# Kernel optimization log

Measured on AMD Instinct MI355X. Metric: run time of the kernel, lower is better.

## Reference

```python
import jax, jax.numpy as jnp
import numpy as np

B, L, D, H, NL, FF, W, V = 4, 8192, 256, 4, 4, 1024, 512, 14
DH = D // H


def _ln(x, g, b, eps=1e-5):
    m = jnp.mean(x, axis=-1, keepdims=True)
    v = jnp.mean((x - m) ** 2, axis=-1, keepdims=True)
    return (x - m) / jnp.sqrt(v + eps) * g + b


def setup_inputs() -> dict:
    key = jax.random.key(0)
    ks = jax.random.split(key, 12)
    s = 0.02
    inp = {
        "byte_ids": jax.random.randint(ks[0], (B, L), 0, V, dtype=jnp.int32),
        "embed": jax.random.normal(ks[1], (V, D), jnp.float32) * s,
        "wq": jax.random.normal(ks[2], (NL, D, D), jnp.float32) * s,
        "bq": jnp.zeros((NL, D), jnp.float32),
        "wk": jax.random.normal(ks[3], (NL, D, D), jnp.float32) * s,
        "bk": jnp.zeros((NL, D), jnp.float32),
        "wv": jax.random.normal(ks[4], (NL, D, D), jnp.float32) * s,
        "bv": jnp.zeros((NL, D), jnp.float32),
        "wo": jax.random.normal(ks[5], (NL, D, D), jnp.float32) * s,
        "bo": jnp.zeros((NL, D), jnp.float32),
        "ln1_g": jnp.ones((NL, D), jnp.float32),
        "ln1_b": jnp.zeros((NL, D), jnp.float32),
        "ln2_g": jnp.ones((NL, D), jnp.float32),
        "ln2_b": jnp.zeros((NL, D), jnp.float32),
        "w1": jax.random.normal(ks[6], (NL, D, FF), jnp.float32) * s,
        "b1": jnp.zeros((NL, FF), jnp.float32),
        "w2": jax.random.normal(ks[7], (NL, FF, D), jnp.float32) * s,
        "b2": jnp.zeros((NL, D), jnp.float32),
        "lnf_g": jnp.ones((D,), jnp.float32),
        "lnf_b": jnp.zeros((D,), jnp.float32),
        "head_w": jax.random.normal(ks[8], (D, V), jnp.float32) * s,
    }
    return inp


def _forward(byte_ids, embed, wq, bq, wk, bk, wv, bv, wo, bo,
             ln1_g, ln1_b, ln2_g, ln2_b, w1, b1, w2, b2, lnf_g, lnf_b, head_w):
    x = embed[byte_ids]                      # [B, L, D]
    nb = L // W                              # number of 512-wide blocks
    scale = 1.0 / np.sqrt(DH)
    # ALiBi slopes: 2^(-8h/H) for h = 1..H
    slopes = jnp.exp2(-8.0 * jnp.arange(1, H + 1, dtype=jnp.float32) / H)
    qi = jnp.arange(W)[:, None]
    ki = jnp.arange(2 * W)[None, :]
    dist = (W + qi - ki).astype(jnp.float32)            # i - j for kv window [prev, cur]
    base = (dist >= 0) & (dist <= W)                    # causal sliding window (left=512)
    mask = jnp.broadcast_to(base, (nb, W, 2 * W))
    mask = mask.at[0].set(base & (ki >= W))             # first block has no previous block
    bias = -slopes[:, None, None] * dist                # [H, W, 2W]

    for l in range(NL):
        h = _ln(x, ln1_g[l], ln1_b[l])
        q = (h @ wq[l] + bq[l]).reshape(B, nb, W, H, DH)
        k = (h @ wk[l] + bk[l]).reshape(B, nb, W, H, DH)
        v = (h @ wv[l] + bv[l]).reshape(B, nb, W, H, DH)
        kp = jnp.pad(k, ((0, 0), (1, 0), (0, 0), (0, 0), (0, 0)))[:, :nb]
        vp = jnp.pad(v, ((0, 0), (1, 0), (0, 0), (0, 0), (0, 0)))[:, :nb]
        kk = jnp.concatenate([kp, k], axis=2)           # [B, nb, 2W, H, DH]
        vv = jnp.concatenate([vp, v], axis=2)
        s = jnp.einsum('bnqhd,bnkhd->bhnqk', q, kk) * scale + bias[None, :, None]
        s = jnp.where(mask[None, None], s, -1e9)
        p = jax.nn.softmax(s, axis=-1)                  # [B, H, nb, W, 2W]
        o = jnp.einsum('bhnqk,bnkhd->bnqhd', p, vv).reshape(B, L, D)
        x = x + o @ wo[l] + bo[l]
        h2 = _ln(x, ln2_g[l], ln2_b[l])
        x = x + jax.nn.gelu(h2 @ w1[l] + b1[l]) @ w2[l] + b2[l]
    x = _ln(x, lnf_g, lnf_b)
    return x @ head_w                                   # [B, L, V]


def reference(byte_ids, embed, wq, bq, wk, bk, wv, bv, wo, bo,
              ln1_g, ln1_b, ln2_g, ln2_b, w1, b1, w2, b2, lnf_g, lnf_b, head_w):
    return _forward(byte_ids, embed, wq, bq, wk, bk, wv, bv, wo, bo,
                    ln1_g, ln1_b, ln2_g, ln2_b, w1, b1, w2, b2, lnf_g, lnf_b, head_w)
```

## Files before the change

### kernel.cpp

```cpp
#include <hip/hip_runtime.h>

#define NLAYER 4
#define M_TOK 32768

typedef unsigned short u16;
typedef __bf16 bf16x8 __attribute__((ext_vector_type(8)));
typedef float f32x4 __attribute__((ext_vector_type(4)));

__device__ inline float bf2f(u16 u) {
    union { unsigned int i; float f; } x; x.i = ((unsigned int)u) << 16; return x.f;
}
__device__ inline u16 f2bf(float f) {
    union { float f; unsigned int i; } x; x.f = f;
    return (u16)((x.i + 0x8000u) >> 16);
}
__device__ inline bf16x8 ld_frag(const u16* p) {
    union { uint4 u; bf16x8 b; } c; c.u = *(const uint4*)p; return c.b;
}
__device__ inline unsigned pk2(float a, float b) {
    union { float f; unsigned i; } ua, ub; ua.f = a; ub.f = b;
    return __builtin_amdgcn_perm(ub.i + 0x8000u, ua.i + 0x8000u, 0x07060302u);
}
__device__ inline float gelu_f(float x) {
    float z = 0.7978845608028654f * (x + 0.044715f * x * x * x);
    float t = 1.f - 2.f / (__expf(2.f * z) + 1.f);
    return 0.5f * x * (1.f + t);
}
__device__ inline void gload_lds16(const u16* g, u16* l) {
    __builtin_amdgcn_global_load_lds(
        (const __attribute__((address_space(1))) unsigned int*)g,
        (__attribute__((address_space(3))) unsigned int*)l, 16, 0, 0);
}

#define BAR()   asm volatile("s_barrier" ::: "memory")
#define WAIT4() asm volatile("s_waitcnt vmcnt(4)" ::: "memory")
#define WAIT0() asm volatile("s_waitcnt vmcnt(0)" ::: "memory")
#define LGKM0() asm volatile("s_waitcnt lgkmcnt(0)" ::: "memory")

__global__ void sniff_kernel(const u16* __restrict__ raw, int* __restrict__ flag)
{
    if (threadIdx.x == 0 && blockIdx.x == 0) {
        int ok = 1;
        for (int i = 0; i < 32; i++) {
            u16 u = raw[i];
            int e = (u >> 7) & 0xFF;
            if (!(u == 0 || (e >= 90 && e <= 140))) ok = 0;
        }
        *flag = ok;
    }
}

struct IngestArgs { const void* src[20]; int off[21]; };
__global__ __launch_bounds__(256) void ingest_all(
    IngestArgs a, float* __restrict__ dst, const int* __restrict__ flag, int tot)
{
    int gid = blockIdx.x * 256 + threadIdx.x;
    if (gid >= tot) return;
    int lo = 0, hi = 20;
    while (hi - lo > 1) { int mid = (lo + hi) >> 1; if (gid >= a.off[mid]) lo = mid; else hi = mid; }
    int local = gid - a.off[lo];
    if (*flag) dst[gid] = bf2f(((const u16*)a.src[lo])[local]);
    else       dst[gid] = ((const float*)a.src[lo])[local];
}

__global__ __launch_bounds__(256) void pack_qkv(
    const float* __restrict__ wq, const float* __restrict__ wk, const float* __restrict__ wv,
    const float* __restrict__ bq, const float* __restrict__ bk, const float* __restrict__ bv,
    u16* __restrict__ wT, float* __restrict__ bT)
{
    int l = blockIdx.y;
    int idx = blockIdx.x * 256 + threadIdx.x;
    int n = idx >> 8, k = idx & 255;
    const float* w = (n < 256) ? wq : (n < 512) ? wk : wv;
    int nn = n & 255;
    wT[(size_t)l * 768 * 256 + idx] = f2bf(w[(size_t)l * 65536 + k * 256 + nn]);
    if (idx < 768) {
        const float* bb = (idx < 256) ? bq : (idx < 512) ? bk : bv;
        bT[l * 768 + idx] = bb[l * 256 + (idx & 255)];
    }
}

__global__ __launch_bounds__(256) void pack_t(
    const float* __restrict__ src, u16* __restrict__ dst, int R, int C)
{
    int l = blockIdx.y;
    int idx = blockIdx.x * 256 + threadIdx.x;
    int c = idx / R, r = idx % R;
    size_t base = (size_t)l * R * C;
    dst[base + idx] = f2bf(src[base + (size_t)r * C + c]);
}

__global__ __launch_bounds__(256) void embed_kernel(
    const int* __restrict__ ids, const float* __restrict__ emb, float* __restrict__ x)
{
    int t = blockIdx.x * 256 + threadIdx.x;
    int row = t >> 6, c = (t & 63) * 4;
    int id = ids[row];
    float4 e = *(const float4*)(emb + (size_t)id * 256 + c);
    *(float4*)(x + (size_t)row * 256 + c) = e;
}

__global__ __launch_bounds__(256) void ln_kernel(
    const float* __restrict__ x, const float* __restrict__ g, const float* __restrict__ b,
    u16* __restrict__ out)
{
    int row = blockIdx.x * 4 + (threadIdx.x >> 6);
    int lane = threadIdx.x & 63;
    float4 v = *(const float4*)(x + (size_t)row * 256 + lane * 4);
    float s = v.x + v.y + v.z + v.w;
    float s2 = v.x * v.x + v.y * v.y + v.z * v.z + v.w * v.w;
    #pragma unroll
    for (int mk = 1; mk < 64; mk <<= 1) {
        s += __shfl_xor(s, mk, 64);
        s2 += __shfl_xor(s2, mk, 64);
    }
    float mean = s * (1.f / 256.f);
    float var = s2 * (1.f / 256.f) - mean * mean;
    float rstd = rsqrtf(var + 1e-5f);
    int d0 = lane * 4;
    float4 gg = *(const float4*)(g + d0);
    float4 bb = *(const float4*)(b + d0);
    union { unsigned long long u; u16 q[4]; } oo;
    oo.q[0] = f2bf((v.x - mean) * rstd * gg.x + bb.x);
    oo.q[1] = f2bf((v.y - mean) * rstd * gg.y + bb.y);
    oo.q[2] = f2bf((v.z - mean) * rstd * gg.z + bb.z);
    oo.q[3] = f2bf((v.w - mean) * rstd * gg.w + bb.w);
    *(unsigned long long*)(out + (size_t)row * 256 + d0) = oo.u;
}

template <int EPI, int K>
__global__ __launch_bounds__(256, 3) void gemm_db(
    const u16* __restrict__ A, const u16* __restrict__ Bt, const float* __restrict__ bias,
    u16* __restrict__ outB, float* __restrict__ resid, int N)
{
    __shared__ u16 lds[17408];
    constexpr int NC = K / 32;
    int tid = threadIdx.x, lane = tid & 63, wave = tid >> 6;
    int col = lane & 15, quad = lane >> 4;
    int wm = (wave >> 1) * 64, wn = (wave & 1) * 64;
    int bm = blockIdx.x * 128, bn = blockIdx.y * 128;

    u16* A0 = lds;          u16* A1 = lds + 4096;
    u16* B0 = lds + 8192;   u16* B1 = lds + 12288;

    int rL = wave * 32 + (lane >> 2);
    int sx = (lane & 3) ^ ((lane >> 2) & 3);
    const u16* srcA0 = A + (size_t)(bm + rL) * K + sx * 8;
    const u16* srcB0 = Bt + (size_t)(bn + rL) * K + sx * 8;
    int st = wave * 1024 + lane * 8;

    int g8 = (quad ^ (col & 3)) * 8;
    int aoff = (wm + col) * 32 + g8;
    int boff = (wn + col) * 32 + g8;

    f32x4 z4 = { 0.f, 0.f, 0.f, 0.f };
    f32x4 acc[4][4];
    #pragma unroll
    for (int i = 0; i < 4; i++)
        #pragma unroll
        for (int j = 0; j < 4; j++) acc[i][j] = z4;

    #define STAGE(c, Ax, Bx) do {                                        \
        const u16* _a = srcA0 + (c) * 32;                                \
        const u16* _b = srcB0 + (c) * 32;                                \
        gload_lds16(_a, (Ax) + st);                                      \
        gload_lds16(_a + (size_t)16 * K, (Ax) + st + 512);               \
        gload_lds16(_b, (Bx) + st);                                      \
        gload_lds16(_b + (size_t)16 * K, (Bx) + st + 512);               \
    } while (0)

    #define CHUNK(Ax, Bx) do {                                           \
        bf16x8 af[4], bfv[4];                                            \
        _Pragma("unroll")                                                \
        for (int i = 0; i < 4; i++) af[i] = ld_frag((Ax) + aoff + i * 512); \
        _Pragma("unroll")                                                \
        for (int j = 0; j < 4; j++) bfv[j] = ld_frag((Bx) + boff + j * 512); \
        _Pragma("unroll")                                                \
        for (int i = 0; i < 4; i++)                                      \
            _Pragma("unroll")                                            \
            for (int j = 0; j < 4; j++)                                  \
                acc[i][j] = __builtin_amdgcn_mfma_f32_16x16x32_bf16(af[i], bfv[j], acc[i][j], 0, 0, 0); \
    } while (0)

    STAGE(0, A0, B0);
    for (int c = 0; c < NC - 2; c += 2) {
        STAGE(c + 1, A1, B1);
        WAIT4(); BAR();
        CHUNK(A0, B0);
        LGKM0(); BAR();
        STAGE(c + 2, A0, B0);
        WAIT4(); BAR();
        CHUNK(A1, B1);
        LGKM0(); BAR();
    }
    STAGE(NC - 1, A1, B1);
    WAIT4(); BAR();
    CHUNK(A0, B0);
    LGKM0(); BAR();
    WAIT0(); BAR();
    CHUNK(A1, B1);
    __syncthreads();

    if (EPI == 2) {
        float* Cf = (float*)lds;
        #pragma unroll
        for (int h = 0; h < 2; h++) {
            if ((wave & 1) == h) {
                #pragma unroll
                for (int j = 0; j < 4; j++) {
                    float bv = bias[bn + wn + j * 16 + col];
                    #pragma unroll
                    for (int i = 0; i < 4; i++) {
                        int rl = wm + i * 16 + quad * 4;
                        #pragma unroll
                        for (int r = 0; r < 4; r++)
                            Cf[(rl + r) * 68 + j * 16 + col] = acc[i][j][r] + bv;
                    }
                }
            }
            LGKM0(); BAR();
            #pragma unroll
            for (int u = 0; u < 8; u++) {
                int row = u * 16 + (tid >> 4);
                int cseg = (tid & 15) * 4;
                float* rp = resid + (size_t)(bm + row) * N + bn + h * 64 + cseg;
                const float* cp = Cf + row * 68 + cseg;
                float4 rv = *(float4*)rp;
                float4 cv = *(const float4*)cp;
                rv.x += cv.x; rv.y += cv.y; rv.z += cv.z; rv.w += cv.w;
                *(float4*)rp = rv;
            }
            LGKM0(); BAR();
        }
    } else {
        u16* Cs = lds;
        #pragma unroll
        for (int j = 0; j < 4; j++) {
            int ccl = wn + j * 16 + col;
            float bv = bias[bn + ccl];
            #pragma unroll
            for (int i = 0; i < 4; i++) {
                int rl = wm + i * 16 + quad * 4;
                #pragma unroll
                for (int r = 0; r < 4; r++) {
                    float v = acc[i][j][r] + bv;
                    if (EPI == 1) v = gelu_f(v);
                    Cs[(rl + r) * 136 + ccl] = f2bf(v);
                }
            }
        }
        __syncthreads();
        #pragma unroll
        for (int u = 0; u < 8; u++) {
            int row = u * 16 + (tid >> 4);
            int c8 = (tid & 15) * 8;
            u16* op = outB + (size_t)(bm + row) * N + bn + c8;
            *(uint4*)op = *(const uint4*)(Cs + row * 136 + c8);
        }
    }
    #undef STAGE
    #undef CHUNK
}

__global__ __launch_bounds__(256, 3) void attn_kernel(
    const u16* __restrict__ qkv, u16* __restrict__ attno)
{
    __shared__ u16 Ks[64 * 72];
    __shared__ u16 Vt[64 * 68];
    __shared__ u16 Ps[4 * 16 * 72];
    int g = blockIdx.x;
    int xc = g & 7, t = g >> 3;
    int r12 = t & 15, s8 = t >> 4;
    int ng = s8 * 8 + xc;
    int bb = ng >> 4, nn = ng & 15;
    int hh = r12 & 3, t2 = r12 >> 2;
    int tid = threadIdx.x, lane = tid & 63, wave = tid >> 6;
    int q16 = lane & 15, quad = lane >> 4;
    float slope = exp2f(-2.f * (float)(hh + 1));
    float slopeL = slope * 1.44269504f;
    const float C1 = 0.125f * 1.44269504f;

    int qt0 = t2 * 2;
    size_t tok0 = (size_t)bb * 8192 + nn * 512;

    bf16x8 bqf[2][2];
    {
        int qrow = t2 * 128 + wave * 16 + q16;
        const u16* qp = qkv + (tok0 + qrow) * 768 + hh * 64 + quad * 8;
        bqf[0][0] = ld_frag(qp);
        bqf[0][1] = ld_frag(qp + 32);
        const u16* qp1 = qp + (size_t)64 * 768;
        bqf[1][0] = ld_frag(qp1);
        bqf[1][1] = ld_frag(qp1 + 32);
    }

    f32x4 z4 = { 0.f, 0.f, 0.f, 0.f };
    f32x4 oa[2][4];
    #pragma unroll
    for (int s = 0; s < 2; s++)
        #pragma unroll
        for (int dt = 0; dt < 4; dt++) oa[s][dt] = z4;
    float lsum[2] = { 0.f, 0.f };
    u16* Psw = Ps + wave * (16 * 72);

    int c_lo = (nn == 0) ? 8 : qt0;
    int c_hi = qt0 + 9;

    int kkK = tid >> 3, c8k = (tid & 7) * 8;
    int kk2 = (tid & 31) * 2, c8v = (tid >> 5) * 8;

    uint4 pk0, pk1, pv0, pv1;
    auto load_c = [&](int c) {
        int tok = (int)tok0 - 512 + c * 64;
        const u16* bK = qkv + (size_t)(tok + kkK) * 768 + hh * 64 + 256 + c8k;
        pk0 = *(const uint4*)bK;
        pk1 = *(const uint4*)(bK + (size_t)32 * 768);
        const u16* bV = qkv + (size_t)(tok + kk2) * 768 + hh * 64 + 512 + c8v;
        pv0 = *(const uint4*)bV;
        pv1 = *(const uint4*)(bV + 768);
    };
    load_c(c_lo);

    for (int c = c_lo; c <= c_hi; ++c) {
        LGKM0(); BAR();
        *(uint4*)(Ks + kkK * 72 + c8k) = pk0;
        *(uint4*)(Ks + (kkK + 32) * 72 + c8k) = pk1;
        {
            union { uint4 u; u16 s[8]; } a, b;
            a.u = pv0; b.u = pv1;
            #pragma unroll
            for (int j = 0; j < 8; j++) {
                unsigned w = (unsigned)a.s[j] | ((unsigned)b.s[j] << 16);
                *(unsigned*)(Vt + (c8v + j) * 68 + kk2) = w;
            }
        }
        if (c < c_hi) load_c(c + 1);
        LGKM0(); BAR();

        bf16x8 kf[4][2];
        #pragma unroll
        for (int kt = 0; kt < 4; kt++)
            #pragma unroll
            for (int ks = 0; ks < 2; ks++)
                kf[kt][ks] = ld_frag(Ks + (kt * 16 + q16) * 72 + ks * 32 + quad * 8);
        bf16x8 vf[4][2];
        #pragma unroll
        for (int dt = 0; dt < 4; dt++)
            #pragma unroll
            for (int ks = 0; ks < 2; ks++) {
                union { uint2 p[2]; bf16x8 b; } cv;
                const u16* vp = Vt + (dt * 16 + q16) * 68 + ks * 32 + quad * 8;
                cv.p[0] = *(const uint2*)(vp);
                cv.p[1] = *(const uint2*)(vp + 4);
                vf[dt][ks] = cv.b;
            }

        int act0 = (c <= qt0 + 8);
        int act1 = (c >= qt0 + 1);
        #pragma unroll
        for (int s = 0; s < 2; s++) {
            if (s == 0 ? !act0 : !act1) continue;
            f32x4 st[4];
            #pragma unroll
            for (int kt = 0; kt < 4; kt++) {
                f32x4 z = z4;
                #pragma unroll
                for (int ks = 0; ks < 2; ks++)
                    z = __builtin_amdgcn_mfma_f32_16x16x32_bf16(kf[kt][ks], bqf[s][ks], z, 0, 0, 0);
                st[kt] = z;
            }
            int qg = t2 * 128 + s * 64 + wave * 16 + q16;
            int D = 512 + qg - c * 64 - quad * 4;
            float nb = -slopeL * (float)D;
            int qts = qt0 + s;
            int diag = (c == qts) || (c == qts + 8);
            float ls = 0.f;
            #pragma unroll
            for (int kt = 0; kt < 4; kt++) {
                float pk[4];
                #pragma unroll
                for (int r = 0; r < 4; r++) {
                    float bias = fmaf(slopeL, (float)(kt * 16 + r), nb);
                    float p = exp2f(fmaf(st[kt][r], C1, bias));
                    if (diag) {
                        int dd = D - (kt * 16 + r);
                        p = ((unsigned)dd <= 512u) ? p : 0.f;
                    }
                    ls += p; pk[r] = p;
                }
                uint2 w;
                w.x = pk2(pk[0], pk[1]);
                w.y = pk2(pk[2], pk[3]);
                *(uint2*)(Psw + q16 * 72 + kt * 16 + quad * 4) = w;
            }
            lsum[s] += ls;
            bf16x8 pf[2];
            #pragma unroll
            for (int ks = 0; ks < 2; ks++)
                pf[ks] = ld_frag(Psw + q16 * 72 + ks * 32 + quad * 8);
            #pragma unroll
            for (int dt = 0; dt < 4; dt++)
                #pragma unroll
                for (int ks = 0; ks < 2; ks++)
                    oa[s][dt] = __builtin_amdgcn_mfma_f32_16x16x32_bf16(pf[ks], vf[dt][ks], oa[s][dt], 0, 0, 0);
        }
    }

    #pragma unroll
    for (int s = 0; s < 2; s++) {
        float lr = lsum[s];
        lr += __shfl_xor(lr, 16, 64);
        lr += __shfl_xor(lr, 32, 64);
        lsum[s] = lr;
    }
    float* lx = (float*)Psw;
    if (quad == 0) { lx[q16] = lsum[0]; lx[16 + q16] = lsum[1]; }
    #pragma unroll
    for (int s = 0; s < 2; s++) {
        float4 lq = *(const float4*)(lx + s * 16 + quad * 4);
        float inv[4] = { 1.f / lq.x, 1.f / lq.y, 1.f / lq.z, 1.f / lq.w };
        int tokb = (int)tok0 + t2 * 128 + s * 64 + wave * 16 + quad * 4;
        #pragma unroll
        for (int r = 0; r < 4; r++)
            #pragma unroll
            for (int dt = 0; dt < 4; dt++)
                attno[(size_t)(tokb + r) * 256 + hh * 64 + dt * 16 + q16] = f2bf(oa[s][dt][r] * inv[r]);
    }
}

__global__ __launch_bounds__(256) void head_ln_kernel(
    const float* __restrict__ x, const float* __restrict__ g, const float* __restrict__ b,
    const float* __restrict__ hw, const int* __restrict__ flag,
    u16* __restrict__ outb, float* __restrict__ outf)
{
    __shared__ float Wt[14 * 256];
    int tid = threadIdx.x;
    for (int i = tid; i < 14 * 256; i += 256) {
        int v = i >> 8, d = i & 255;
        Wt[i] = hw[d * 14 + v];
    }
    __syncthreads();
    int wave = tid >> 6, lane = tid & 63;
    int row = blockIdx.x * 4 + wave;
    float4 v = *(const float4*)(x + (size_t)row * 256 + lane * 4);
    float s = v.x + v.y + v.z + v.w;
    float s2 = v.x * v.x + v.y * v.y + v.z * v.z + v.w * v.w;
    #pragma unroll
    for (int mk = 1; mk < 64; mk <<= 1) {
        s += __shfl_xor(s, mk, 64);
        s2 += __shfl_xor(s2, mk, 64);
    }
    float mean = s * (1.f / 256.f);
    float var = s2 * (1.f / 256.f) - mean * mean;
    float rstd = rsqrtf(var + 1e-5f);
    int d0 = lane * 4;
    float4 gg = *(const float4*)(g + d0);
    float4 bb = *(const float4*)(b + d0);
    float hv[4];
    hv[0] = (v.x - mean) * rstd * gg.x + bb.x;
    hv[1] = (v.y - mean) * rstd * gg.y + bb.y;
    hv[2] = (v.z - mean) * rstd * gg.z + bb.z;
    hv[3] = (v.w - mean) * rstd * gg.w + bb.w;
    int isbf = *flag;
    for (int vv = 0; vv < 14; vv++) {
        float4 wv4 = *(const float4*)(Wt + vv * 256 + lane * 4);
        float sd = hv[0] * wv4.x + hv[1] * wv4.y + hv[2] * wv4.z + hv[3] * wv4.w;
        #pragma unroll
        for (int mk = 1; mk < 64; mk <<= 1) sd += __shfl_xor(sd, mk, 64);
        if (lane == 0) {
            if (isbf) outb[(size_t)row * 14 + vv] = f2bf(sd);
            else      outf[(size_t)row * 14 + vv] = sd;
        }
    }
}

extern "C" void kernel_launch(void* const* d_in, const int* in_sizes, int n_in,
                              void* d_out, int out_size, void* d_ws, size_t ws_size,
                              hipStream_t stream) {
    (void)out_size; (void)ws_size;
    const int* ids = (const int*)d_in[0];

    char* ws = (char*)d_ws;
    int* flag = (int*)ws; ws += 16;

    IngestArgs ia;
    int off = 0;
    for (int i = 1; i < n_in && i <= 20; i++) {
        ia.src[i - 1] = d_in[i];
        ia.off[i - 1] = off;
        off += in_sizes[i];
    }
    ia.off[20] = off;
    float* fbase = (float*)ws;
    ws += (size_t)((off + 3) & ~3) * 4;
    float* fin[21];
    for (int i = 1; i <= 20; i++) fin[i] = fbase + ia.off[i - 1];

    float* x    = (float*)ws;  ws += (size_t)M_TOK * 256 * 4;
    u16* h      = (u16*)ws;    ws += (size_t)M_TOK * 256 * 2;
    u16* qkv    = (u16*)ws;    ws += (size_t)M_TOK * 768 * 2;
    u16* attno  = (u16*)ws;    ws += (size_t)M_TOK * 256 * 2;
    u16* ff     = (u16*)ws;    ws += (size_t)M_TOK * 1024 * 2;
    u16* wqkvT  = (u16*)ws;    ws += (size_t)NLAYER * 768 * 256 * 2;
    u16* woT    = (u16*)ws;    ws += (size_t)NLAYER * 256 * 256 * 2;
    u16* w1T    = (u16*)ws;    ws += (size_t)NLAYER * 1024 * 256 * 2;
    u16* w2T    = (u16*)ws;    ws += (size_t)NLAYER * 256 * 1024 * 2;
    float* bqkv = (float*)ws;  ws += (size_t)NLAYER * 768 * 4;

    sniff_kernel<<<1, 64, 0, stream>>>((const u16*)d_in[1], flag);
    ingest_all<<<(off + 255) / 256, 256, 0, stream>>>(ia, fbase, flag, off);

    pack_qkv<<<dim3(768, NLAYER), 256, 0, stream>>>(fin[2], fin[4], fin[6],
                                                    fin[3], fin[5], fin[7], wqkvT, bqkv);
    pack_t<<<dim3(256, NLAYER), 256, 0, stream>>>(fin[8], woT, 256, 256);
    pack_t<<<dim3(1024, NLAYER), 256, 0, stream>>>(fin[14], w1T, 256, 1024);
    pack_t<<<dim3(1024, NLAYER), 256, 0, stream>>>(fin[16], w2T, 1024, 256);

    embed_kernel<<<8192, 256, 0, stream>>>(ids, fin[1], x);

    for (int l = 0; l < NLAYER; ++l) {
        ln_kernel<<<8192, 256, 0, stream>>>(x, fin[10] + l * 256, fin[11] + l * 256, h);
        gemm_db<0, 256><<<dim3(256, 6), 256, 0, stream>>>(h, wqkvT + (size_t)l * 768 * 256,
                                                          bqkv + l * 768, qkv, nullptr, 768);
        attn_kernel<<<1024, 256, 0, stream>>>(qkv, attno);
        gemm_db<2, 256><<<dim3(256, 2), 256, 0, stream>>>(attno, woT + (size_t)l * 65536,
                                                          fin[9] + l * 256, nullptr, x, 256);
        ln_kernel<<<8192, 256, 0, stream>>>(x, fin[12] + l * 256, fin[13] + l * 256, h);
        gemm_db<1, 256><<<dim3(256, 8), 256, 0, stream>>>(h, w1T + (size_t)l * 262144,
                                                          fin[15] + l * 1024, ff, nullptr, 1024);
        gemm_db<2, 1024><<<dim3(256, 2), 256, 0, stream>>>(ff, w2T + (size_t)l * 262144,
                                                           fin[17] + l * 256, nullptr, x, 256);
    }
    head_ln_kernel<<<8192, 256, 0, stream>>>(x, fin[18], fin[19], fin[20], flag,
                                             (u16*)d_out, (float*)d_out);
}
```

Before: 1.050 ms.

## Replace LDS double-buffered GEMM with direct global-to-register fragment loads

```diff
diff --git a/kernel.cpp b/kernel.cpp
--- a/kernel.cpp
+++ b/kernel.cpp
@@ -26,15 +26,8 @@
     float t = 1.f - 2.f / (__expf(2.f * z) + 1.f);
     return 0.5f * x * (1.f + t);
 }
-__device__ inline void gload_lds16(const u16* g, u16* l) {
-    __builtin_amdgcn_global_load_lds(
-        (const __attribute__((address_space(1))) unsigned int*)g,
-        (__attribute__((address_space(3))) unsigned int*)l, 16, 0, 0);
-}
 
 #define BAR()   asm volatile("s_barrier" ::: "memory")
-#define WAIT4() asm volatile("s_waitcnt vmcnt(4)" ::: "memory")
-#define WAIT0() asm volatile("s_waitcnt vmcnt(0)" ::: "memory")
 #define LGKM0() asm volatile("s_waitcnt lgkmcnt(0)" ::: "memory")
 
 __global__ void sniff_kernel(const u16* __restrict__ raw, int* __restrict__ flag)
@@ -129,29 +122,24 @@
 }
 
 template <int EPI, int K>
-__global__ __launch_bounds__(256, 3) void gemm_db(
+__global__ __launch_bounds__(256, 3) void gemm_reg(
     const u16* __restrict__ A, const u16* __restrict__ Bt, const float* __restrict__ bias,
     u16* __restrict__ outB, float* __restrict__ resid, int N)
 {
     __shared__ u16 lds[17408];
-    constexpr int NC = K / 32;
     int tid = threadIdx.x, lane = tid & 63, wave = tid >> 6;
     int col = lane & 15, quad = lane >> 4;
     int wm = (wave >> 1) * 64, wn = (wave & 1) * 64;
     int bm = blockIdx.x * 128, bn = blockIdx.y * 128;
 
-    u16* A0 = lds;          u16* A1 = lds + 4096;
-    u16* B0 = lds + 8192;   u16* B1 = lds + 12288;
-
-    int rL = wave * 32 + (lane >> 2);
-    int sx = (lane & 3) ^ ((lane >> 2) & 3);
-    const u16* srcA0 = A + (size_t)(bm + rL) * K + sx * 8;
-    const u16* srcB0 = Bt + (size_t)(bn + rL) * K + sx * 8;
-    int st = wave * 1024 + lane * 8;
-
-    int g8 = (quad ^ (col & 3)) * 8;
-    int aoff = (wm + col) * 32 + g8;
-    int boff = (wn + col) * 32 + g8;
+    const u16* ap[4];
+    const u16* bp[4];
+    #pragma unroll
+    for (int i = 0; i < 4; i++)
+        ap[i] = A + (size_t)(bm + wm + i * 16 + col) * K + quad * 8;
+    #pragma unroll
+    for (int j = 0; j < 4; j++)
+        bp[j] = Bt + (size_t)(bn + wn + j * 16 + col) * K + quad * 8;
 
     f32x4 z4 = { 0.f, 0.f, 0.f, 0.f };
     f32x4 acc[4][4];
@@ -160,46 +148,19 @@
         #pragma unroll
         for (int j = 0; j < 4; j++) acc[i][j] = z4;
 
-    #define STAGE(c, Ax, Bx) do {                                        \
-        const u16* _a = srcA0 + (c) * 32;                                \
-        const u16* _b = srcB0 + (c) * 32;                                \
-        gload_lds16(_a, (Ax) + st);                                      \
-        gload_lds16(_a + (size_t)16 * K, (Ax) + st + 512);               \
-        gload_lds16(_b, (Bx) + st);                                      \
-        gload_lds16(_b + (size_t)16 * K, (Bx) + st + 512);               \
-    } while (0)
-
-    #define CHUNK(Ax, Bx) do {                                           \
-        bf16x8 af[4], bfv[4];                                            \
-        _Pragma("unroll")                                                \
-        for (int i = 0; i < 4; i++) af[i] = ld_frag((Ax) + aoff + i * 512); \
-        _Pragma("unroll")                                                \
-        for (int j = 0; j < 4; j++) bfv[j] = ld_frag((Bx) + boff + j * 512); \
-        _Pragma("unroll")                                                \
-        for (int i = 0; i < 4; i++)                                      \
-            _Pragma("unroll")                                            \
-            for (int j = 0; j < 4; j++)                                  \
-                acc[i][j] = __builtin_amdgcn_mfma_f32_16x16x32_bf16(af[i], bfv[j], acc[i][j], 0, 0, 0); \
-    } while (0)
-
-    STAGE(0, A0, B0);
-    for (int c = 0; c < NC - 2; c += 2) {
-        STAGE(c + 1, A1, B1);
-        WAIT4(); BAR();
-        CHUNK(A0, B0);
-        LGKM0(); BAR();
-        STAGE(c + 2, A0, B0);
-        WAIT4(); BAR();
-        CHUNK(A1, B1);
-        LGKM0(); BAR();
-    }
-    STAGE(NC - 1, A1, B1);
-    WAIT4(); BAR();
-    CHUNK(A0, B0);
-    LGKM0(); BAR();
-    WAIT0(); BAR();
-    CHUNK(A1, B1);
-    __syncthreads();
+    #pragma unroll
+    for (int ks = 0; ks < K / 32; ks++) {
+        bf16x8 af[4], bfv[4];
+        #pragma unroll
+        for (int i = 0; i < 4; i++) af[i] = ld_frag(ap[i] + ks * 32);
+        #pragma unroll
+        for (int j = 0; j < 4; j++) bfv[j] = ld_frag(bp[j] + ks * 32);
+        #pragma unroll
+        for (int i = 0; i < 4; i++)
+            #pragma unroll
+            for (int j = 0; j < 4; j++)
+                acc[i][j] = __builtin_amdgcn_mfma_f32_16x16x32_bf16(af[i], bfv[j], acc[i][j], 0, 0, 0);
+    }
 
     if (EPI == 2) {
         float* Cf = (float*)lds;
@@ -258,8 +219,6 @@
             *(uint4*)op = *(const uint4*)(Cs + row * 136 + c8);
         }
     }
-    #undef STAGE
-    #undef CHUNK
 }
 
 __global__ __launch_bounds__(256, 3) void attn_kernel(
@@ -520,16 +479,16 @@
 
     for (int l = 0; l < NLAYER; ++l) {
         ln_kernel<<<8192, 256, 0, stream>>>(x, fin[10] + l * 256, fin[11] + l * 256, h);
-        gemm_db<0, 256><<<dim3(256, 6), 256, 0, stream>>>(h, wqkvT + (size_t)l * 768 * 256,
-                                                          bqkv + l * 768, qkv, nullptr, 768);
+        gemm_reg<0, 256><<<dim3(256, 6), 256, 0, stream>>>(h, wqkvT + (size_t)l * 768 * 256,
+                                                           bqkv + l * 768, qkv, nullptr, 768);
         attn_kernel<<<1024, 256, 0, stream>>>(qkv, attno);
-        gemm_db<2, 256><<<dim3(256, 2), 256, 0, stream>>>(attno, woT + (size_t)l * 65536,
-                                                          fin[9] + l * 256, nullptr, x, 256);
+        gemm_reg<2, 256><<<dim3(256, 2), 256, 0, stream>>>(attno, woT + (size_t)l * 65536,
+                                                           fin[9] + l * 256, nullptr, x, 256);
         ln_kernel<<<8192, 256, 0, stream>>>(x, fin[12] + l * 256, fin[13] + l * 256, h);
-        gemm_db<1, 256><<<dim3(256, 8), 256, 0, stream>>>(h, w1T + (size_t)l * 262144,
-                                                          fin[15] + l * 1024, ff, nullptr, 1024);
-        gemm_db<2, 1024><<<dim3(256, 2), 256, 0, stream>>>(ff, w2T + (size_t)l * 262144,
-                                                           fin[17] + l * 256, nullptr, x, 256);
+        gemm_reg<1, 256><<<dim3(256, 8), 256, 0, stream>>>(h, w1T + (size_t)l * 262144,
+                                                           fin[15] + l * 1024, ff, nullptr, 1024);
+        gemm_reg<2, 1024><<<dim3(256, 2), 256, 0, stream>>>(ff, w2T + (size_t)l * 262144,
+                                                            fin[17] + l * 256, nullptr, x, 256);
     }
     head_ln_kernel<<<8192, 256, 0, stream>>>(x, fin[18], fin[19], fin[20], flag,
                                              (u16*)d_out, (float*)d_out);
```

Result: slower. 1.350 ms (+28.6%).

## Fuse FFN up-projection, GELU and down-projection into one MLP kernel

Applied to the files above, without the earlier changes.

```diff
diff --git a/kernel.cpp b/kernel.cpp
--- a/kernel.cpp
+++ b/kernel.cpp
@@ -260,6 +260,169 @@
     }
     #undef STAGE
     #undef CHUNK
+}
+
+__global__ __launch_bounds__(512, 2) void mlp_kernel(
+    const u16* __restrict__ Ain, const u16* __restrict__ w1T, const u16* __restrict__ w2T,
+    const float* __restrict__ b1, const float* __restrict__ b2, float* __restrict__ xr)
+{
+    __shared__ u16 As[32768];
+    __shared__ u16 Ws[32768];
+    __shared__ u16 Gs[16384];
+
+    int tid = threadIdx.x, lane = tid & 63, wave = tid >> 6;
+    int col = lane & 15, quad = lane >> 4;
+    int wq = wave & 3, wh = wave >> 2;
+    int wm2 = wh * 64;
+    int bm = blockIdx.x * 128;
+    int g8 = (quad ^ (col & 3)) * 8;
+    int gx8 = (col & 7) * 8;
+    int sx = (lane & 3) ^ ((lane >> 2) & 3);
+    int st = wave * 512 + lane * 8;
+    int aoffB = (wm2 + col) * 32 + g8;
+    int bw1off = (wq * 16 + col) * 32 + g8;
+    int wn2off = (wq * 64 + col) * 32 + g8;
+    int wn1c = wq * 16 + col;
+
+    float b1r[16], b2r[4];
+    {
+        int c0 = wq * 16 + col;
+        #pragma unroll
+        for (int f = 0; f < 8; f++) {
+            b1r[f * 2 + 0] = b1[f * 128 + c0];
+            b1r[f * 2 + 1] = b1[f * 128 + 64 + c0];
+        }
+        #pragma unroll
+        for (int j = 0; j < 4; j++) b2r[j] = b2[wq * 64 + j * 16 + col];
+    }
+
+    f32x4 z4 = { 0.f, 0.f, 0.f, 0.f };
+    f32x4 acc2[4][4];
+    #pragma unroll
+    for (int i = 0; i < 4; i++)
+        #pragma unroll
+        for (int j = 0; j < 4; j++) acc2[i][j] = z4;
+
+    #define STAGE_W1(ff, hh, WB) do {                                               \
+        const u16* _s = w1T + (size_t)((ff) * 128 + (hh) * 64 + wq * 16 + (lane >> 2)) * 256 + sx * 8; \
+        _Pragma("unroll")                                                           \
+        for (int i_ = 0; i_ < 4; i_++)                                              \
+            gload_lds16(_s + (i_ * 2 + wh) * 32, (WB) + i_ * 4096 + st);            \
+    } while (0)
+
+    #define STAGE_W2(ff, kh, WB) do {                                               \
+        _Pragma("unroll")                                                           \
+        for (int i_ = 0; i_ < 4; i_++) {                                            \
+            int _rv = (i_ & 1) * 128 + wave * 16 + (lane >> 2);                     \
+            gload_lds16(w2T + (size_t)_rv * 1024 + (ff) * 128 + (kh) * 64 + (i_ >> 1) * 32 + sx * 8, \
+                        (WB) + (i_ >> 1) * 8192 + (i_ & 1) * 4096 + st);            \
+        }                                                                           \
+    } while (0)
+
+    #define G1_PHASE(ff, hh, WB) do {                                               \
+        f32x4 a1[4]; a1[0] = z4; a1[1] = z4; a1[2] = z4; a1[3] = z4;                \
+        _Pragma("unroll")                                                           \
+        for (int ks = 0; ks < 8; ks++) {                                            \
+            bf16x8 bw = ld_frag((WB) + ks * 2048 + bw1off);                         \
+            _Pragma("unroll")                                                       \
+            for (int i = 0; i < 4; i++) {                                           \
+                bf16x8 av = ld_frag(As + ks * 4096 + aoffB + i * 512);              \
+                a1[i] = __builtin_amdgcn_mfma_f32_16x16x32_bf16(av, bw, a1[i], 0, 0, 0); \
+            }                                                                       \
+        }                                                                           \
+        float bv = b1r[(ff) * 2 + (hh)];                                            \
+        _Pragma("unroll")                                                           \
+        for (int i = 0; i < 4; i++) {                                               \
+            _Pragma("unroll")                                                       \
+            for (int r = 0; r < 4; r++) {                                           \
+                int row = wm2 + i * 16 + quad * 4 + r;                              \
+                float vv = gelu_f(a1[i][r] + bv);                                   \
+                Gs[row * 128 + (((hh) * 64 + wn1c) ^ ((row & 7) * 8))] = f2bf(vv);  \
+            }                                                                       \
+        }                                                                           \
+    } while (0)
+
+    #define G2_PHASE(kh, WB) do {                                                   \
+        _Pragma("unroll")                                                           \
+        for (int ks = 0; ks < 2; ks++) {                                            \
+            bf16x8 gf[4], wf[4];                                                    \
+            _Pragma("unroll")                                                       \
+            for (int i = 0; i < 4; i++)                                             \
+                gf[i] = ld_frag(Gs + (wm2 + i * 16 + col) * 128 +                   \
+                                (((kh) * 64 + ks * 32 + quad * 8) ^ gx8));          \
+            _Pragma("unroll")                                                       \
+            for (int j = 0; j < 4; j++)                                             \
+                wf[j] = ld_frag((WB) + ks * 8192 + wn2off + j * 512);               \
+            _Pragma("unroll")                                                       \
+            for (int i = 0; i < 4; i++)                                             \
+                _Pragma("unroll")                                                   \
+                for (int j = 0; j < 4; j++)                                         \
+                    acc2[i][j] = __builtin_amdgcn_mfma_f32_16x16x32_bf16(gf[i], wf[j], acc2[i][j], 0, 0, 0); \
+        }                                                                           \
+    } while (0)
+
+    {
+        const u16* sA = Ain + (size_t)(bm + wave * 16 + (lane >> 2)) * 256 + sx * 8;
+        #pragma unroll
+        for (int c = 0; c < 8; c++) gload_lds16(sA + c * 32, As + c * 4096 + st);
+    }
+    STAGE_W1(0, 0, Ws);
+    STAGE_W1(0, 1, Ws + 16384);
+    WAIT4(); BAR();
+
+    for (int f = 0; f < 8; ++f) {
+        G1_PHASE(f, 0, Ws);
+        LGKM0(); BAR();
+        STAGE_W2(f, 0, Ws);
+        WAIT4(); BAR();
+        G1_PHASE(f, 1, Ws + 16384);
+        LGKM0(); BAR();
+        STAGE_W2(f, 1, Ws + 16384);
+        WAIT4(); BAR();
+        G2_PHASE(0, Ws);
+        BAR();
+        if (f < 7) { STAGE_W1(f + 1, 0, Ws); WAIT4(); } else WAIT0();
+        BAR();
+        G2_PHASE(1, Ws + 16384);
+        BAR();
+        if (f < 7) { STAGE_W1(f + 1, 1, Ws + 16384); WAIT4(); }
+        BAR();
+    }
+
+    float* Cf = (float*)As;
+    #pragma unroll
+    for (int h = 0; h < 4; h++) {
+        if (wq == h) {
+            #pragma unroll
+            for (int j = 0; j < 4; j++) {
+                float bv = b2r[j];
+                #pragma unroll
+                for (int i = 0; i < 4; i++) {
+                    int rl = wm2 + i * 16 + quad * 4;
+                    #pragma unroll
+                    for (int r = 0; r < 4; r++)
+                        Cf[(rl + r) * 68 + j * 16 + col] = acc2[i][j][r] + bv;
+                }
+            }
+        }
+        LGKM0(); BAR();
+        #pragma unroll
+        for (int u = 0; u < 4; u++) {
+            int row = u * 32 + (tid >> 4);
+            int cseg = (tid & 15) * 4;
+            float* rp = xr + (size_t)(bm + row) * 256 + h * 64 + cseg;
+            const float* cp = Cf + row * 68 + cseg;
+            float4 rv = *(float4*)rp;
+            float4 cv = *(const float4*)cp;
+            rv.x += cv.x; rv.y += cv.y; rv.z += cv.z; rv.w += cv.w;
+            *(float4*)rp = rv;
+        }
+        LGKM0(); BAR();
+    }
+    #undef STAGE_W1
+    #undef STAGE_W2
+    #undef G1_PHASE
+    #undef G2_PHASE
 }
 
 __global__ __launch_bounds__(256, 3) void attn_kernel(
@@ -500,7 +663,6 @@
     u16* h      = (u16*)ws;    ws += (size_t)M_TOK * 256 * 2;
     u16* qkv    = (u16*)ws;    ws += (size_t)M_TOK * 768 * 2;
     u16* attno  = (u16*)ws;    ws += (size_t)M_TOK * 256 * 2;
-    u16* ff     = (u16*)ws;    ws += (size_t)M_TOK * 1024 * 2;
     u16* wqkvT  = (u16*)ws;    ws += (size_t)NLAYER * 768 * 256 * 2;
     u16* woT    = (u16*)ws;    ws += (size_t)NLAYER * 256 * 256 * 2;
     u16* w1T    = (u16*)ws;    ws += (size_t)NLAYER * 1024 * 256 * 2;
@@ -526,10 +688,9 @@
         gemm_db<2, 256><<<dim3(256, 2), 256, 0, stream>>>(attno, woT + (size_t)l * 65536,
                                                           fin[9] + l * 256, nullptr, x, 256);
         ln_kernel<<<8192, 256, 0, stream>>>(x, fin[12] + l * 256, fin[13] + l * 256, h);
-        gemm_db<1, 256><<<dim3(256, 8), 256, 0, stream>>>(h, w1T + (size_t)l * 262144,
-                                                          fin[15] + l * 1024, ff, nullptr, 1024);
-        gemm_db<2, 1024><<<dim3(256, 2), 256, 0, stream>>>(ff, w2T + (size_t)l * 262144,
-                                                           fin[17] + l * 256, nullptr, x, 256);
+        mlp_kernel<<<256, 512, 0, stream>>>(h, w1T + (size_t)l * 262144,
+                                            w2T + (size_t)l * 262144,
+                                            fin[15] + l * 1024, fin[17] + l * 256, x);
     }
     head_ln_kernel<<<8192, 256, 0, stream>>>(x, fin[18], fin[19], fin[20], flag,
                                              (u16*)d_out, (float*)d_out);
```

Result: faster. 983.8 us (-6.3%).

## Fuse MLP up and down projections into a producer-consumer kernel

Applied to the files above, without the earlier changes.

```diff
diff --git a/kernel.cpp b/kernel.cpp
--- a/kernel.cpp
+++ b/kernel.cpp
@@ -260,6 +260,143 @@
     }
     #undef STAGE
     #undef CHUNK
+}
+
+__global__ __launch_bounds__(1024, 4) void mlp_pc(
+    const u16* __restrict__ hin, const u16* __restrict__ w1T, const u16* __restrict__ w2T,
+    const float* __restrict__ b1, const float* __restrict__ b2, float* __restrict__ xr)
+{
+    __shared__ u16 L[81920];
+    int tid = threadIdx.x, lane = tid & 63, wave = tid >> 6;
+    int colL = lane & 15, quad = lane >> 4;
+    int sx = (lane & 3) ^ ((lane >> 2) & 3);
+    int bm = blockIdx.x * 128;
+    int isG1 = (wave < 8);
+
+    int c0 = wave >> 2;
+    int nb1 = (wave & 3) * 16;
+    const u16* w1s = w1T + (size_t)(nb1 + (lane >> 2)) * 256 + sx * 8;
+    int w1d = c0 * 2048 + nb1 * 32 + lane * 8;
+    const u16* w2s = w2T + (size_t)(wave * 16 + (lane >> 2)) * 1024 + sx * 8;
+    int w2d = wave * 512 + lane * 8;
+
+    int wnh = wave & 1, wmg = (wave >> 1) & 3;
+    int gw = wave & 7, gr = gw >> 2, gc = gw & 3;
+    int swzA = (quad ^ (colL & 3)) * 8;
+
+    f32x4 z4 = { 0.f, 0.f, 0.f, 0.f };
+    f32x4 acc2[4][4];
+    #pragma unroll
+    for (int i = 0; i < 4; i++)
+        #pragma unroll
+        for (int j = 0; j < 4; j++) acc2[i][j] = z4;
+
+    #define STAGE_W1(ff, base) do {                                   \
+        const u16* _s = w1s + (size_t)(ff) * 16384;                   \
+        gload_lds16(_s + c0 * 32, L + (base) + w1d);                  \
+        gload_lds16(_s + (c0 + 4) * 32, L + (base) + 8192 + w1d);     \
+    } while (0)
+
+    #define STAGE_W2(ff, base) do {                                   \
+        const u16* _s = w2s + (ff) * 64;                              \
+        gload_lds16(_s, L + (base) + w2d);                            \
+        gload_lds16(_s + 32, L + (base) + 8192 + w2d);                \
+    } while (0)
+
+    #define G2_BODY(gbase, wbase) do {                                               \
+        const u16* _g = L + (gbase);                                                 \
+        const u16* _w = L + (wbase);                                                 \
+        _Pragma("unroll")                                                            \
+        for (int ks = 0; ks < 2; ks++) {                                             \
+            bf16x8 gf[4], wf[4];                                                     \
+            _Pragma("unroll")                                                        \
+            for (int i = 0; i < 4; i++) {                                            \
+                int row = gr * 64 + i * 16 + colL;                                   \
+                gf[i] = ld_frag(_g + row * 64 + (((ks * 4 + quad) ^ (colL & 7)) * 8)); \
+            }                                                                        \
+            _Pragma("unroll")                                                        \
+            for (int j = 0; j < 4; j++)                                              \
+                wf[j] = ld_frag(_w + ks * 8192 + (gc * 64 + j * 16 + colL) * 32 + swzA); \
+            _Pragma("unroll")                                                        \
+            for (int i = 0; i < 4; i++)                                              \
+                _Pragma("unroll")                                                    \
+                for (int j = 0; j < 4; j++)                                          \
+                    acc2[i][j] = __builtin_amdgcn_mfma_f32_16x16x32_bf16(gf[i], wf[j], acc2[i][j], 0, 0, 0); \
+        }                                                                            \
+    } while (0)
+
+    STAGE_W1(0, 16384);
+
+    for (int f = 0; f < 16; ++f) {
+        int pc = f & 1, pn = pc ^ 1;
+        STAGE_W1((f < 15) ? (f + 1) : 15, 16384 + pn * 16384);
+        STAGE_W2(f, 49152 + pc * 16384);
+        WAIT4(); BAR();
+        if (isG1) {
+            const u16* w1c = L + 16384 + pc * 16384;
+            float b1v[2][4];
+            #pragma unroll
+            for (int i = 0; i < 2; i++)
+                #pragma unroll
+                for (int r = 0; r < 4; r++)
+                    b1v[i][r] = b1[f * 64 + wnh * 32 + i * 16 + quad * 4 + r];
+            f32x4 a1[2][2];
+            a1[0][0] = z4; a1[0][1] = z4; a1[1][0] = z4; a1[1][1] = z4;
+            const u16* ap0 = hin + (size_t)(bm + wmg * 32 + colL) * 256 + quad * 8;
+            const u16* ap1 = ap0 + (size_t)16 * 256;
+            #pragma unroll
+            for (int ks = 0; ks < 8; ks++) {
+                bf16x8 wf0 = ld_frag(w1c + ks * 2048 + (wnh * 32 + colL) * 32 + swzA);
+                bf16x8 wf1 = ld_frag(w1c + ks * 2048 + (wnh * 32 + 16 + colL) * 32 + swzA);
+                bf16x8 am0 = ld_frag(ap0 + ks * 32);
+                bf16x8 am1 = ld_frag(ap1 + ks * 32);
+                a1[0][0] = __builtin_amdgcn_mfma_f32_16x16x32_bf16(wf0, am0, a1[0][0], 0, 0, 0);
+                a1[0][1] = __builtin_amdgcn_mfma_f32_16x16x32_bf16(wf0, am1, a1[0][1], 0, 0, 0);
+                a1[1][0] = __builtin_amdgcn_mfma_f32_16x16x32_bf16(wf1, am0, a1[1][0], 0, 0, 0);
+                a1[1][1] = __builtin_amdgcn_mfma_f32_16x16x32_bf16(wf1, am1, a1[1][1], 0, 0, 0);
+            }
+            u16* gdst = L + pc * 8192;
+            #pragma unroll
+            for (int i = 0; i < 2; i++)
+                #pragma unroll
+                for (int jm = 0; jm < 2; jm++) {
+                    int m = wmg * 32 + jm * 16 + colL;
+                    int m7 = m & 7;
+                    #pragma unroll
+                    for (int rp = 0; rp < 2; rp++) {
+                        int n = wnh * 32 + i * 16 + quad * 4 + rp * 2;
+                        float v0 = gelu_f(a1[i][jm][rp * 2] + b1v[i][rp * 2]);
+                        float v1 = gelu_f(a1[i][jm][rp * 2 + 1] + b1v[i][rp * 2 + 1]);
+                        unsigned pw = pk2(v0, v1);
+                        *(unsigned*)(gdst + m * 64 + (((n >> 3) ^ m7) * 8) + (n & 7)) = pw;
+                    }
+                }
+        } else if (f > 0) {
+            G2_BODY(pn * 8192, 49152 + pn * 16384);
+        }
+        LGKM0(); BAR();
+    }
+
+    WAIT0(); BAR();
+    if (!isG1) {
+        G2_BODY(8192, 65536);
+        float b2v[4];
+        #pragma unroll
+        for (int j = 0; j < 4; j++) b2v[j] = b2[gc * 64 + j * 16 + colL];
+        #pragma unroll
+        for (int i = 0; i < 4; i++)
+            #pragma unroll
+            for (int j = 0; j < 4; j++)
+                #pragma unroll
+                for (int r = 0; r < 4; r++) {
+                    int row = bm + gr * 64 + i * 16 + quad * 4 + r;
+                    float* p = xr + (size_t)row * 256 + gc * 64 + j * 16 + colL;
+                    *p += acc2[i][j][r] + b2v[j];
+                }
+    }
+    #undef STAGE_W1
+    #undef STAGE_W2
+    #undef G2_BODY
 }
 
 __global__ __launch_bounds__(256, 3) void attn_kernel(
@@ -500,7 +637,6 @@
     u16* h      = (u16*)ws;    ws += (size_t)M_TOK * 256 * 2;
     u16* qkv    = (u16*)ws;    ws += (size_t)M_TOK * 768 * 2;
     u16* attno  = (u16*)ws;    ws += (size_t)M_TOK * 256 * 2;
-    u16* ff     = (u16*)ws;    ws += (size_t)M_TOK * 1024 * 2;
     u16* wqkvT  = (u16*)ws;    ws += (size_t)NLAYER * 768 * 256 * 2;
     u16* woT    = (u16*)ws;    ws += (size_t)NLAYER * 256 * 256 * 2;
     u16* w1T    = (u16*)ws;    ws += (size_t)NLAYER * 1024 * 256 * 2;
@@ -526,10 +662,9 @@
         gemm_db<2, 256><<<dim3(256, 2), 256, 0, stream>>>(attno, woT + (size_t)l * 65536,
                                                           fin[9] + l * 256, nullptr, x, 256);
         ln_kernel<<<8192, 256, 0, stream>>>(x, fin[12] + l * 256, fin[13] + l * 256, h);
-        gemm_db<1, 256><<<dim3(256, 8), 256, 0, stream>>>(h, w1T + (size_t)l * 262144,
-                                                          fin[15] + l * 1024, ff, nullptr, 1024);
-        gemm_db<2, 1024><<<dim3(256, 2), 256, 0, stream>>>(ff, w2T + (size_t)l * 262144,
-                                                           fin[17] + l * 256, nullptr, x, 256);
+        mlp_pc<<<256, 1024, 0, stream>>>(h, w1T + (size_t)l * 262144,
+                                         w2T + (size_t)l * 262144,
+                                         fin[15] + l * 1024, fin[17] + l * 256, x);
     }
     head_ln_kernel<<<8192, 256, 0, stream>>>(x, fin[18], fin[19], fin[20], flag,
                                              (u16*)d_out, (float*)d_out);
```

After: 1.227 ms. 1.17x slower.
